# Kernel optimization log

Measured on AMD Instinct MI355X. Metric: run time of the kernel, lower is better.

## Reference

```python
import jax, jax.numpy as jnp
import numpy as np

B, S, D, H = 4, 2048, 1024, 16
DH = D // H
DFF = 4 * D
EPS = 1e-7


def _layernorm(x, scale, shift):
    # Note original quirk: (normalized + shift) * scale, biased variance, eps=1e-7
    m = jnp.mean(x, axis=-1, keepdims=True)
    v = jnp.mean((x - m) ** 2, axis=-1, keepdims=True)
    return ((x - m) / jnp.sqrt(v + EPS) + shift) * scale


def _gelu(x):
    c = jnp.sqrt(jnp.asarray(2.0 / jnp.pi, dtype=x.dtype))
    return 0.5 * x * (1.0 + jnp.tanh(c * (x + 0.044715 * x ** 3)))


def setup_inputs() -> dict:
    key = jax.random.key(0)
    ks = jax.random.split(key, 8)
    s = 0.02
    return {
        "x": jax.random.normal(ks[0], (B, S, D), jnp.float32),
        "Wq": jax.random.normal(ks[1], (D, D), jnp.float32) * s,
        "Wk": jax.random.normal(ks[2], (D, D), jnp.float32) * s,
        "Wv": jax.random.normal(ks[3], (D, D), jnp.float32) * s,
        "Wo": jax.random.normal(ks[4], (D, D), jnp.float32) * s,
        "bo": jnp.zeros((D,), jnp.float32),
        "W1": jax.random.normal(ks[5], (DFF, D), jnp.float32) * s,
        "b1": jnp.zeros((DFF,), jnp.float32),
        "W2": jax.random.normal(ks[6], (D, DFF), jnp.float32) * s,
        "b2": jnp.zeros((D,), jnp.float32),
        "ln1_scale": jnp.ones((D,), jnp.float32),
        "ln1_shift": jnp.zeros((D,), jnp.float32),
        "ln2_scale": jnp.ones((D,), jnp.float32),
        "ln2_shift": jnp.zeros((D,), jnp.float32),
    }


def reference(x, Wq, Wk, Wv, Wo, bo, W1, b1, W2, b2,
              ln1_scale, ln1_shift, ln2_scale, ln2_shift):
    b, s, d = x.shape
    h = _layernorm(x, ln1_scale, ln1_shift)
    # torch Linear: y = h @ W.T
    q = (h @ Wq.T).reshape(b, s, H, DH).transpose(0, 2, 1, 3)  # bhsd
    k = (h @ Wk.T).reshape(b, s, H, DH).transpose(0, 2, 1, 3)
    v = (h @ Wv.T).reshape(b, s, H, DH).transpose(0, 2, 1, 3)
    scores = jnp.einsum('bhqd,bhkd->bhqk', q, k) / jnp.sqrt(jnp.asarray(DH, x.dtype))
    causal = jnp.tril(jnp.ones((s, s), dtype=bool))
    scores = jnp.where(causal, scores, -jnp.inf)
    attn = jax.nn.softmax(scores, axis=-1)
    ctx = jnp.einsum('bhqk,bhkd->bhqd', attn, v)
    ctx = ctx.transpose(0, 2, 1, 3).reshape(b, s, d)
    attn_out = ctx @ Wo.T + bo
    x1 = x + attn_out  # residual (dropout is identity at eval / p effectively unused)
    h2 = _layernorm(x1, ln2_scale, ln2_shift)
    ff = _gelu(h2 @ W1.T + b1) @ W2.T + b2
    return x1 + ff
```

## Files before the change

kernel.cpp:

```cpp
#include <hip/hip_runtime.h>
#include <hip/hip_bf16.h>
#include <math.h>

typedef __bf16 bf16;
typedef __bf16 bf16x2_t __attribute__((ext_vector_type(2)));
typedef __bf16 bf16x4_t __attribute__((ext_vector_type(4)));
typedef __bf16 bf16x8_t __attribute__((ext_vector_type(8)));
typedef float  floatx4  __attribute__((ext_vector_type(4)));

#define DEVI static __device__ __forceinline__

constexpr int Bb = 4, Ss = 2048, Dd = 1024, Hh = 16, DHh = 64, DFFc = 4096;
constexpr int NTOK = Bb * Ss;
constexpr int NQKV = 3072;

DEVI void gld_lds16(const void* g, void* l) {
  __builtin_amdgcn_global_load_lds(
      (const __attribute__((address_space(1))) void*)g,
      (__attribute__((address_space(3))) void*)l, 16, 0, 0);
}

DEVI float gelu_f(float x) {
  const float c = 0.7978845608028654f;
  float t = tanhf(c * (x + 0.044715f * x * x * x));
  return 0.5f * x * (1.0f + t);
}

DEVI int xcd_lin(int lin, int nwg) {
  return (lin & 7) * (nwg >> 3) + (lin >> 3);
}

struct CastArgs {
  const float* src[6];
  bf16* dst[6];
  int n[6];
};
__global__ __launch_bounds__(256) void cast_w_kernel(CastArgs a) {
  const int which = blockIdx.y;
  const int idx = (blockIdx.x * 256 + threadIdx.x) * 4;
  if (idx >= a.n[which]) return;
  float4 v = *(const float4*)(a.src[which] + idx);
  bf16x4_t o = {(bf16)v.x, (bf16)v.y, (bf16)v.z, (bf16)v.w};
  *(bf16x4_t*)(a.dst[which] + idx) = o;
}

template <typename TIN>
__global__ __launch_bounds__(256) void ln_kernel(const TIN* __restrict__ x,
                                                 const float* __restrict__ sc,
                                                 const float* __restrict__ sh,
                                                 bf16* __restrict__ out) {
  __shared__ float rs[4], rs2[4];
  const int row = blockIdx.x, t = threadIdx.x;
  const TIN* xr = x + (size_t)row * Dd;
  float v[4];
  if constexpr (sizeof(TIN) == 2) {
    bf16x4_t tmp = *(const bf16x4_t*)((const bf16*)xr + t * 4);
#pragma unroll
    for (int i = 0; i < 4; i++) v[i] = (float)tmp[i];
  } else {
    float4 tmp = *(const float4*)((const float*)xr + t * 4);
    v[0] = tmp.x; v[1] = tmp.y; v[2] = tmp.z; v[3] = tmp.w;
  }
  float s = v[0] + v[1] + v[2] + v[3];
  float s2 = v[0] * v[0] + v[1] * v[1] + v[2] * v[2] + v[3] * v[3];
#pragma unroll
  for (int off = 1; off < 64; off <<= 1) {
    s += __shfl_xor(s, off);
    s2 += __shfl_xor(s2, off);
  }
  if ((t & 63) == 0) { rs[t >> 6] = s; rs2[t >> 6] = s2; }
  __syncthreads();
  float S1 = rs[0] + rs[1] + rs[2] + rs[3];
  float S2 = rs2[0] + rs2[1] + rs2[2] + rs2[3];
  float mean = S1 * (1.0f / Dd);
  float var = S2 * (1.0f / Dd) - mean * mean;
  float rinv = rsqrtf(var + 1e-7f);
#pragma unroll
  for (int i = 0; i < 4; i++) {
    int c = t * 4 + i;
    out[(size_t)row * Dd + c] = (bf16)(((v[i] - mean) * rinv + sh[c]) * sc[c]);
  }
}

template <int MODE>
__global__ __launch_bounds__(512, 2) void gemm8(const bf16* __restrict__ A,
                                                const bf16* __restrict__ Bw,
                                                const float* __restrict__ bias,
                                                const void* __restrict__ res,
                                                void* __restrict__ outp,
                                                int M, int N, int K) {
  constexpr int ABUF = 16384;
  constexpr int BBUF = 8192;
  __shared__ bf16 lds[3 * (ABUF + BBUF)];
  bf16* Ab = lds;
  bf16* Bb = lds + 3 * ABUF;

  const int tid = threadIdx.x;
  const int w = tid >> 6, lane = tid & 63;
  const int quad = lane >> 4, l16 = lane & 15;
  const int l7x8 = (lane & 7) << 3;
  const int wr = w >> 1, wc = w & 1;

  const int gx = (int)gridDim.x;
  const int nwg = gx * (int)gridDim.y;
  const int lin = xcd_lin((int)blockIdx.y * gx + (int)blockIdx.x, nwg);
  const int m0 = (lin / gx) * 256;
  const int n0 = (lin % gx) * 128;

  const int s0 = w * 1024 + lane * 16;
  const int sr = s0 >> 7;
  const int sc = ((s0 ^ ((sr & 7) << 4)) & 127) >> 1;
  const int toff = w * 512 + lane * 8;

  const bf16* Ag[2][2];
  const bf16* Bg[2];
#pragma unroll
  for (int h = 0; h < 2; h++)
#pragma unroll
    for (int j = 0; j < 2; j++)
      Ag[h][j] = A + (size_t)(m0 + h * 128 + j * 64 + sr) * K + sc;
#pragma unroll
  for (int j = 0; j < 2; j++)
    Bg[j] = Bw + (size_t)(n0 + j * 64 + sr) * K + sc;

  auto issue = [&](int kofs, int s) {
#pragma unroll
    for (int h = 0; h < 2; h++)
#pragma unroll
      for (int j = 0; j < 2; j++)
        gld_lds16(Ag[h][j] + kofs, Ab + s * ABUF + h * 8192 + j * 4096 + toff);
#pragma unroll
    for (int j = 0; j < 2; j++)
      gld_lds16(Bg[j] + kofs, Bb + s * BBUF + j * 4096 + toff);
  };

  const int abase = (wr * 64 + l16) * 64 + quad * 8;
  const int bbase = (wc * 64 + l16) * 64 + quad * 8;

  floatx4 acc[4][4] = {};

  const int NT = K >> 6;
  issue(0, 0);
  issue(64, 1);

  for (int t = 0; t < NT; ++t) {
    const int s = t % 3;
    if (t < NT - 1) {
      asm volatile("s_waitcnt vmcnt(6)" ::: "memory");
    } else {
      asm volatile("s_waitcnt vmcnt(0)" ::: "memory");
    }
    __builtin_amdgcn_sched_barrier(0);
    __builtin_amdgcn_s_barrier();
    __builtin_amdgcn_sched_barrier(0);
    if (t + 2 < NT) issue((t + 2) * 64, (t + 2) % 3);

    const bf16* aB = Ab + s * ABUF;
    const bf16* bB = Bb + s * BBUF;
    bf16x8_t bfr[4][2];
#pragma unroll
    for (int p = 0; p < 2; ++p) {
      bf16x8_t af[2][2];
#pragma unroll
      for (int im = 0; im < 2; ++im)
#pragma unroll
        for (int kk = 0; kk < 2; ++kk)
          af[im][kk] = *(const bf16x8_t*)(
              aB + ((abase + (p * 2 + im) * 1024 + kk * 32) ^ l7x8));
      if (p == 0) {
#pragma unroll
        for (int j2 = 0; j2 < 4; ++j2)
#pragma unroll
          for (int kk = 0; kk < 2; ++kk)
            bfr[j2][kk] = *(const bf16x8_t*)(
                bB + ((bbase + j2 * 1024 + kk * 32) ^ l7x8));
      }
      __builtin_amdgcn_s_barrier();
      __builtin_amdgcn_sched_barrier(0);
      __builtin_amdgcn_s_setprio(1);
#pragma unroll
      for (int im = 0; im < 2; ++im)
#pragma unroll
        for (int j2 = 0; j2 < 4; ++j2)
#pragma unroll
          for (int kk = 0; kk < 2; ++kk)
            acc[p * 2 + im][j2] = __builtin_amdgcn_mfma_f32_16x16x32_bf16(
                af[im][kk], bfr[j2][kk], acc[p * 2 + im][j2], 0, 0, 0);
      __builtin_amdgcn_s_setprio(0);
      if (p == 0) {
        __builtin_amdgcn_s_barrier();
        __builtin_amdgcn_sched_barrier(0);
      }
    }
  }

#pragma unroll
  for (int i = 0; i < 4; ++i) {
    const int rbase = m0 + wr * 64 + i * 16 + quad * 4;
#pragma unroll
    for (int j2 = 0; j2 < 4; ++j2) {
      const int col = n0 + wc * 64 + j2 * 16 + l16;
      float bv = 0.f;
      if constexpr (MODE == 1 || MODE == 2 || MODE == 3) bv = bias[col];
#pragma unroll
      for (int r = 0; r < 4; ++r) {
        const int row = rbase + r;
        float vacc = acc[i][j2][r] + bv;
        if constexpr (MODE == 0) {
          ((bf16*)outp)[(size_t)row * N + col] = (bf16)vacc;
        } else if constexpr (MODE == 1) {
          float xres = ((const float*)res)[(size_t)row * N + col];
          ((bf16*)outp)[(size_t)row * N + col] = (bf16)(xres + vacc);
        } else if constexpr (MODE == 2) {
          ((bf16*)outp)[(size_t)row * N + col] = (bf16)gelu_f(vacc);
        } else {
          float xres = (float)((const bf16*)res)[(size_t)row * N + col];
          ((float*)outp)[(size_t)row * N + col] = xres + vacc;
        }
      }
    }
  }
}

__global__ __launch_bounds__(256) void attn_kernel(const bf16* __restrict__ QKV,
                                                   bf16* __restrict__ ctx) {
  __shared__ bf16 Ks[64 * 72];
  __shared__ bf16 Vt[64 * 72];
  __shared__ bf16 Ps[4][16 * 72];

  const int tid = threadIdx.x;
  const int wave = tid >> 6, lane = tid & 63;
  const int quad = lane >> 4, l16 = lane & 15;
  const int lin = xcd_lin((int)blockIdx.y * 16 + (int)blockIdx.x, 16 * Bb * Hh);
  const int qb = lin & 15;
  const int bh = lin >> 4;
  const int bsel = bh >> 4, hsel = bh & 15;
  const size_t base = ((size_t)bsel * Ss) * NQKV + (size_t)hsel * 64;
  const bf16* Qp = QKV + base;
  const bf16* Kp = QKV + base + 1024;
  const bf16* Vp = QKV + base + 2048;

  const int kr0 = tid >> 3, kc0 = (tid & 7) * 8;
  const int vp2 = tid & 31, vs = tid >> 5;

  for (int t = 0; t < 2; t++) {
    const int qt = (t == 0) ? qb : 31 - qb;
    const int q0 = qt * 64;

    const int qrow = q0 + wave * 16 + l16;
    bf16x8_t qf0 = *(const bf16x8_t*)(Qp + (size_t)qrow * NQKV + quad * 8);
    bf16x8_t qf1 = *(const bf16x8_t*)(Qp + (size_t)qrow * NQKV + 32 + quad * 8);
#pragma unroll
    for (int i = 0; i < 8; i++) {
      qf0[i] = (bf16)((float)qf0[i] * 0.125f);
      qf1[i] = (bf16)((float)qf1[i] * 0.125f);
    }

    floatx4 o[4] = {};
    float l_i[4] = {0.f, 0.f, 0.f, 0.f};

    {
      bf16x8_t k0 = *(const bf16x8_t*)(Kp + (size_t)kr0 * NQKV + kc0);
      bf16x8_t k1 = *(const bf16x8_t*)(Kp + (size_t)(kr0 + 32) * NQKV + kc0);
      const bf16* v0p = Vp + (size_t)(2 * vp2) * NQKV + vs * 8;
      bf16x8_t va = *(const bf16x8_t*)(v0p);
      bf16x8_t vb = *(const bf16x8_t*)(v0p + NQKV);
      *(bf16x8_t*)(Ks + kr0 * 72 + kc0) = k0;
      *(bf16x8_t*)(Ks + (kr0 + 32) * 72 + kc0) = k1;
#pragma unroll
      for (int i = 0; i < 8; i++) {
        bf16x2_t p2 = {va[i], vb[i]};
        *(bf16x2_t*)(Vt + (vs * 8 + i) * 72 + 2 * vp2) = p2;
      }
      __syncthreads();
    }

    const int ntiles = qt + 1;
    for (int it = 0; it < ntiles; ++it) {
      const int kc = it * 64;
      const bool more = (it + 1) < ntiles;

      bf16x8_t nk0, nk1, nva, nvb;
      if (more) {
        const int kn = kc + 64;
        nk0 = *(const bf16x8_t*)(Kp + (size_t)(kn + kr0) * NQKV + kc0);
        nk1 = *(const bf16x8_t*)(Kp + (size_t)(kn + kr0 + 32) * NQKV + kc0);
        const bf16* v0p = Vp + (size_t)(kn + 2 * vp2) * NQKV + vs * 8;
        nva = *(const bf16x8_t*)(v0p);
        nvb = *(const bf16x8_t*)(v0p + NQKV);
      }

      floatx4 sg[4];
      __builtin_amdgcn_s_setprio(1);
#pragma unroll
      for (int g = 0; g < 4; g++) {
        floatx4 s = {0.f, 0.f, 0.f, 0.f};
        bf16x8_t ka = *(const bf16x8_t*)(Ks + (g * 16 + l16) * 72 + quad * 8);
        bf16x8_t kb = *(const bf16x8_t*)(Ks + (g * 16 + l16) * 72 + 32 + quad * 8);
        s = __builtin_amdgcn_mfma_f32_16x16x32_bf16(qf0, ka, s, 0, 0, 0);
        s = __builtin_amdgcn_mfma_f32_16x16x32_bf16(qf1, kb, s, 0, 0, 0);
        sg[g] = s;
      }
      __builtin_amdgcn_s_setprio(0);

      bf16* pw = &Ps[wave][0];
      const bool diag = (kc == q0);
      if (diag) {
#pragma unroll
        for (int r = 0; r < 4; r++) {
          const int rq = q0 + wave * 16 + quad * 4 + r;
          float p[4];
          float rsum = 0.f;
#pragma unroll
          for (int g = 0; g < 4; g++) {
            float v = (kc + g * 16 + l16 > rq) ? -1e30f : sg[g][r];
            p[g] = __expf(v);
            rsum += p[g];
          }
          rsum += __shfl_xor(rsum, 1);
          rsum += __shfl_xor(rsum, 2);
          rsum += __shfl_xor(rsum, 4);
          rsum += __shfl_xor(rsum, 8);
          l_i[r] += rsum;
#pragma unroll
          for (int g = 0; g < 4; g++)
            pw[(quad * 4 + r) * 72 + g * 16 + l16] = (bf16)p[g];
        }
      } else {
#pragma unroll
        for (int r = 0; r < 4; r++) {
          float p[4];
          float rsum = 0.f;
#pragma unroll
          for (int g = 0; g < 4; g++) {
            p[g] = __expf(sg[g][r]);
            rsum += p[g];
          }
          rsum += __shfl_xor(rsum, 1);
          rsum += __shfl_xor(rsum, 2);
          rsum += __shfl_xor(rsum, 4);
          rsum += __shfl_xor(rsum, 8);
          l_i[r] += rsum;
#pragma unroll
          for (int g = 0; g < 4; g++)
            pw[(quad * 4 + r) * 72 + g * 16 + l16] = (bf16)p[g];
        }
      }

      bf16x8_t pf0 = *(const bf16x8_t*)(pw + l16 * 72 + quad * 8);
      bf16x8_t pf1 = *(const bf16x8_t*)(pw + l16 * 72 + 32 + quad * 8);
      __builtin_amdgcn_s_setprio(1);
#pragma unroll
      for (int nt = 0; nt < 4; nt++) {
        bf16x8_t vf0 = *(const bf16x8_t*)(Vt + (nt * 16 + l16) * 72 + quad * 8);
        bf16x8_t vf1 = *(const bf16x8_t*)(Vt + (nt * 16 + l16) * 72 + 32 + quad * 8);
        o[nt] = __builtin_amdgcn_mfma_f32_16x16x32_bf16(pf0, vf0, o[nt], 0, 0, 0);
        o[nt] = __builtin_amdgcn_mfma_f32_16x16x32_bf16(pf1, vf1, o[nt], 0, 0, 0);
      }
      __builtin_amdgcn_s_setprio(0);

      __syncthreads();
      if (more) {
        *(bf16x8_t*)(Ks + kr0 * 72 + kc0) = nk0;
        *(bf16x8_t*)(Ks + (kr0 + 32) * 72 + kc0) = nk1;
#pragma unroll
        for (int i = 0; i < 8; i++) {
          bf16x2_t p2 = {nva[i], nvb[i]};
          *(bf16x2_t*)(Vt + (vs * 8 + i) * 72 + 2 * vp2) = p2;
        }
        __syncthreads();
      }
    }

#pragma unroll
    for (int nt = 0; nt < 4; nt++)
#pragma unroll
      for (int r = 0; r < 4; r++) {
        const int rq = q0 + wave * 16 + quad * 4 + r;
        size_t a = ((size_t)bsel * Ss + rq) * Dd + (size_t)hsel * DHh + nt * 16 + l16;
        ctx[a] = (bf16)(o[nt][r] / l_i[r]);
      }
  }
}

extern "C" void kernel_launch(void* const* d_in, const int* in_sizes, int n_in,
                              void* d_out, int out_size, void* d_ws, size_t ws_size,
                              hipStream_t stream) {
  (void)in_sizes; (void)n_in; (void)out_size; (void)ws_size;
  const float* x = (const float*)d_in[0];
  const float* Wq = (const float*)d_in[1];
  const float* Wk = (const float*)d_in[2];
  const float* Wv = (const float*)d_in[3];
  const float* Wo = (const float*)d_in[4];
  const float* bo = (const float*)d_in[5];
  const float* W1 = (const float*)d_in[6];
  const float* b1 = (const float*)d_in[7];
  const float* W2 = (const float*)d_in[8];
  const float* b2 = (const float*)d_in[9];
  const float* ln1s = (const float*)d_in[10];
  const float* ln1b = (const float*)d_in[11];
  const float* ln2s = (const float*)d_in[12];
  const float* ln2b = (const float*)d_in[13];

  char* wsb = (char*)d_ws;
  const size_t MB = 1024 * 1024;
  bf16* Wqb = (bf16*)(wsb);
  bf16* Wkb = (bf16*)(wsb + 2 * MB);
  bf16* Wvb = (bf16*)(wsb + 4 * MB);
  bf16* Wob = (bf16*)(wsb + 6 * MB);
  bf16* W1b = (bf16*)(wsb + 8 * MB);
  bf16* W2b = (bf16*)(wsb + 16 * MB);
  bf16* h   = (bf16*)(wsb + 24 * MB);
  bf16* qkv = (bf16*)(wsb + 40 * MB);
  bf16* ctx = (bf16*)(wsb + 88 * MB);
  bf16* x1  = (bf16*)(wsb + 104 * MB);
  bf16* h2  = ctx;
  bf16* ff1 = h;

  dim3 blk(256, 1, 1);
  dim3 blk8(512, 1, 1);

  CastArgs ca;
  ca.src[0] = Wq; ca.src[1] = Wk; ca.src[2] = Wv; ca.src[3] = Wo;
  ca.src[4] = W1; ca.src[5] = W2;
  ca.dst[0] = Wqb; ca.dst[1] = Wkb; ca.dst[2] = Wvb; ca.dst[3] = Wob;
  ca.dst[4] = W1b; ca.dst[5] = W2b;
  ca.n[0] = ca.n[1] = ca.n[2] = ca.n[3] = Dd * Dd;
  ca.n[4] = ca.n[5] = Dd * DFFc;
  cast_w_kernel<<<dim3((Dd * DFFc) / (256 * 4), 6, 1), blk, 0, stream>>>(ca);

  ln_kernel<float><<<dim3(NTOK, 1, 1), blk, 0, stream>>>(x, ln1s, ln1b, h);
  gemm8<0><<<dim3(24, NTOK / 256, 1), blk8, 0, stream>>>(h, Wqb, nullptr, nullptr,
                                                         qkv, NTOK, NQKV, Dd);
  attn_kernel<<<dim3(16, Bb * Hh, 1), blk, 0, stream>>>(qkv, ctx);
  gemm8<1><<<dim3(8, NTOK / 256, 1), blk8, 0, stream>>>(ctx, Wob, bo, x, x1,
                                                        NTOK, Dd, Dd);
  ln_kernel<bf16><<<dim3(NTOK, 1, 1), blk, 0, stream>>>(x1, ln2s, ln2b, h2);
  gemm8<2><<<dim3(32, NTOK / 256, 1), blk8, 0, stream>>>(h2, W1b, b1, nullptr, ff1,
                                                         NTOK, DFFc, Dd);
  gemm8<3><<<dim3(8, NTOK / 256, 1), blk8, 0, stream>>>(ff1, W2b, b2, x1,
                                                        (float*)d_out, NTOK, Dd, DFFc);
}
```

Measured before the change: 530.4 us.

## Template GEMM on tile width, use 256x256 tiles and split-phase double buffering

The GEMM kernel is templated on the N tile width. The QKV and FFN1 projections now use 256x256 block tiles with a 2x4 warp layout, which raises data reuse per loaded tile and halves the grid. LDS buffering drops from three stages to two, and global-to-LDS loads are split into halves issued at different phases of the MFMA loop, with waitcnt and barriers placed so that prefetch overlaps compute. The larger tiles raise LDS and register pressure and leave fewer workgroups to spread across CUs.

```diff
diff --git a/kernel.cpp b/kernel.cpp
--- a/kernel.cpp
+++ b/kernel.cpp
@@ -82,98 +82,111 @@
   }
 }
 
-template <int MODE>
-__global__ __launch_bounds__(512, 2) void gemm8(const bf16* __restrict__ A,
+template <int BN, int MODE>
+__global__ __launch_bounds__(512, 2) void gemmk(const bf16* __restrict__ A,
                                                 const bf16* __restrict__ Bw,
                                                 const float* __restrict__ bias,
                                                 const void* __restrict__ res,
                                                 void* __restrict__ outp,
                                                 int M, int N, int K) {
-  constexpr int ABUF = 16384;
-  constexpr int BBUF = 8192;
-  __shared__ bf16 lds[3 * (ABUF + BBUF)];
+  constexpr int BUNITS = BN / 64;
+  constexpr int AELEM = 16384;
+  constexpr int BELEM = BUNITS * 4096;
+  constexpr int WN = (BN == 256) ? 4 : 2;
+  constexpr int WM = 8 / WN;
+  constexpr int WR_H = 256 / WM;
+  constexpr int M_rep = WR_H / 16;
+  constexpr int NPH = M_rep / 2;
+  __shared__ bf16 lds[2 * (AELEM + BELEM)];
   bf16* Ab = lds;
-  bf16* Bb = lds + 3 * ABUF;
+  bf16* Bl = lds + 2 * AELEM;
 
   const int tid = threadIdx.x;
   const int w = tid >> 6, lane = tid & 63;
   const int quad = lane >> 4, l16 = lane & 15;
   const int l7x8 = (lane & 7) << 3;
-  const int wr = w >> 1, wc = w & 1;
+  const int wr = w / WN, wc = w % WN;
 
   const int gx = (int)gridDim.x;
   const int nwg = gx * (int)gridDim.y;
   const int lin = xcd_lin((int)blockIdx.y * gx + (int)blockIdx.x, nwg);
   const int m0 = (lin / gx) * 256;
-  const int n0 = (lin % gx) * 128;
+  const int n0 = (lin % gx) * BN;
 
   const int s0 = w * 1024 + lane * 16;
   const int sr = s0 >> 7;
   const int sc = ((s0 ^ ((sr & 7) << 4)) & 127) >> 1;
   const int toff = w * 512 + lane * 8;
 
-  const bf16* Ag[2][2];
-  const bf16* Bg[2];
-#pragma unroll
-  for (int h = 0; h < 2; h++)
-#pragma unroll
-    for (int j = 0; j < 2; j++)
-      Ag[h][j] = A + (size_t)(m0 + h * 128 + j * 64 + sr) * K + sc;
-#pragma unroll
-  for (int j = 0; j < 2; j++)
-    Bg[j] = Bw + (size_t)(n0 + j * 64 + sr) * K + sc;
-
-  auto issue = [&](int kofs, int s) {
-#pragma unroll
-    for (int h = 0; h < 2; h++)
-#pragma unroll
-      for (int j = 0; j < 2; j++)
-        gld_lds16(Ag[h][j] + kofs, Ab + s * ABUF + h * 8192 + j * 4096 + toff);
-#pragma unroll
-    for (int j = 0; j < 2; j++)
-      gld_lds16(Bg[j] + kofs, Bb + s * BBUF + j * 4096 + toff);
+  const bf16* Agu[4];
+  const bf16* Bgu[BUNITS];
+#pragma unroll
+  for (int u = 0; u < 4; ++u) Agu[u] = A + (size_t)(m0 + u * 64 + sr) * K + sc;
+#pragma unroll
+  for (int u = 0; u < BUNITS; ++u)
+    Bgu[u] = Bw + (size_t)(n0 + u * 64 + sr) * K + sc;
+
+  auto issA = [&](int t, int lo) {
+    const int q = t & 1, ko = t * 64;
+#pragma unroll
+    for (int u = 0; u < 2; ++u)
+      gld_lds16(Agu[lo + u] + ko, Ab + q * AELEM + (lo + u) * 4096 + toff);
   };
-
-  const int abase = (wr * 64 + l16) * 64 + quad * 8;
-  const int bbase = (wc * 64 + l16) * 64 + quad * 8;
-
-  floatx4 acc[4][4] = {};
-
+  auto issB = [&](int t, int lo, int cnt) {
+    const int q = t & 1, ko = t * 64;
+#pragma unroll 2
+    for (int u = 0; u < cnt; ++u)
+      gld_lds16(Bgu[lo + u] + ko, Bl + q * BELEM + (lo + u) * 4096 + toff);
+  };
+
+  auto rdA = [&](int q, int mi, int kk) {
+    const int r = wr * WR_H + mi * 16 + l16;
+    return *(const bf16x8_t*)(Ab + q * AELEM + (r >> 6) * 4096 + (r & 63) * 64 +
+                              ((quad * 8 + kk * 32) ^ l7x8));
+  };
+  auto rdB = [&](int q, int j, int kk) {
+    const int r = wc * 64 + j * 16 + l16;
+    return *(const bf16x8_t*)(Bl + q * BELEM + (r >> 6) * 4096 + (r & 63) * 64 +
+                              ((quad * 8 + kk * 32) ^ l7x8));
+  };
+
+  floatx4 acc[M_rep][4] = {};
   const int NT = K >> 6;
-  issue(0, 0);
-  issue(64, 1);
+
+  issA(0, 0); issA(0, 2); issB(0, 0, BUNITS);
+  issA(1, 0);
+  if (BN == 256) {
+    issB(1, 0, 2);
+    asm volatile("s_waitcnt vmcnt(4)" ::: "memory");
+  } else {
+    asm volatile("s_waitcnt vmcnt(2)" ::: "memory");
+  }
+  __builtin_amdgcn_sched_barrier(0);
+  __builtin_amdgcn_s_barrier();
+  __builtin_amdgcn_sched_barrier(0);
 
   for (int t = 0; t < NT; ++t) {
-    const int s = t % 3;
-    if (t < NT - 1) {
-      asm volatile("s_waitcnt vmcnt(6)" ::: "memory");
-    } else {
-      asm volatile("s_waitcnt vmcnt(0)" ::: "memory");
-    }
-    __builtin_amdgcn_sched_barrier(0);
-    __builtin_amdgcn_s_barrier();
-    __builtin_amdgcn_sched_barrier(0);
-    if (t + 2 < NT) issue((t + 2) * 64, (t + 2) % 3);
-
-    const bf16* aB = Ab + s * ABUF;
-    const bf16* bB = Bb + s * BBUF;
-    bf16x8_t bfr[4][2];
-#pragma unroll
-    for (int p = 0; p < 2; ++p) {
+    const int q = t & 1;
+    bf16x8_t bfv[4][2];
+#pragma unroll
+    for (int p = 0; p < NPH; ++p) {
       bf16x8_t af[2][2];
 #pragma unroll
       for (int im = 0; im < 2; ++im)
 #pragma unroll
         for (int kk = 0; kk < 2; ++kk)
-          af[im][kk] = *(const bf16x8_t*)(
-              aB + ((abase + (p * 2 + im) * 1024 + kk * 32) ^ l7x8));
+          af[im][kk] = rdA(q, p * 2 + im, kk);
       if (p == 0) {
 #pragma unroll
-        for (int j2 = 0; j2 < 4; ++j2)
+        for (int j = 0; j < 4; ++j)
 #pragma unroll
           for (int kk = 0; kk < 2; ++kk)
-            bfr[j2][kk] = *(const bf16x8_t*)(
-                bB + ((bbase + j2 * 1024 + kk * 32) ^ l7x8));
+            bfv[j][kk] = rdB(q, j, kk);
+        if (t + 1 < NT) {
+          issA(t + 1, 2);
+          if (BN == 256) issB(t + 1, 2, 2);
+          else issB(t + 1, 0, 2);
+        }
       }
       __builtin_amdgcn_s_barrier();
       __builtin_amdgcn_sched_barrier(0);
@@ -181,22 +194,31 @@
 #pragma unroll
       for (int im = 0; im < 2; ++im)
 #pragma unroll
-        for (int j2 = 0; j2 < 4; ++j2)
+        for (int j = 0; j < 4; ++j)
 #pragma unroll
           for (int kk = 0; kk < 2; ++kk)
-            acc[p * 2 + im][j2] = __builtin_amdgcn_mfma_f32_16x16x32_bf16(
-                af[im][kk], bfr[j2][kk], acc[p * 2 + im][j2], 0, 0, 0);
+            acc[p * 2 + im][j] = __builtin_amdgcn_mfma_f32_16x16x32_bf16(
+                af[im][kk], bfv[j][kk], acc[p * 2 + im][j], 0, 0, 0);
       __builtin_amdgcn_s_setprio(0);
-      if (p == 0) {
-        __builtin_amdgcn_s_barrier();
+      if (p == NPH - 1) {
+        if (t + 2 < NT) {
+          issA(t + 2, 0);
+          if (BN == 256) issB(t + 2, 0, 2);
+          if (BN == 256) asm volatile("s_waitcnt vmcnt(4)" ::: "memory");
+          else           asm volatile("s_waitcnt vmcnt(2)" ::: "memory");
+        } else {
+          asm volatile("s_waitcnt vmcnt(0)" ::: "memory");
+        }
         __builtin_amdgcn_sched_barrier(0);
       }
+      __builtin_amdgcn_s_barrier();
+      __builtin_amdgcn_sched_barrier(0);
     }
   }
 
 #pragma unroll
-  for (int i = 0; i < 4; ++i) {
-    const int rbase = m0 + wr * 64 + i * 16 + quad * 4;
+  for (int i = 0; i < M_rep; ++i) {
+    const int rbase = m0 + wr * WR_H + i * 16 + quad * 4;
 #pragma unroll
     for (int j2 = 0; j2 < 4; ++j2) {
       const int col = n0 + wc * 64 + j2 * 16 + l16;
@@ -430,14 +452,14 @@
   cast_w_kernel<<<dim3((Dd * DFFc) / (256 * 4), 6, 1), blk, 0, stream>>>(ca);
 
   ln_kernel<float><<<dim3(NTOK, 1, 1), blk, 0, stream>>>(x, ln1s, ln1b, h);
-  gemm8<0><<<dim3(24, NTOK / 256, 1), blk8, 0, stream>>>(h, Wqb, nullptr, nullptr,
-                                                         qkv, NTOK, NQKV, Dd);
+  gemmk<256, 0><<<dim3(12, NTOK / 256, 1), blk8, 0, stream>>>(h, Wqb, nullptr, nullptr,
+                                                              qkv, NTOK, NQKV, Dd);
   attn_kernel<<<dim3(16, Bb * Hh, 1), blk, 0, stream>>>(qkv, ctx);
-  gemm8<1><<<dim3(8, NTOK / 256, 1), blk8, 0, stream>>>(ctx, Wob, bo, x, x1,
-                                                        NTOK, Dd, Dd);
+  gemmk<128, 1><<<dim3(8, NTOK / 256, 1), blk8, 0, stream>>>(ctx, Wob, bo, x, x1,
+                                                             NTOK, Dd, Dd);
   ln_kernel<bf16><<<dim3(NTOK, 1, 1), blk, 0, stream>>>(x1, ln2s, ln2b, h2);
-  gemm8<2><<<dim3(32, NTOK / 256, 1), blk8, 0, stream>>>(h2, W1b, b1, nullptr, ff1,
-                                                         NTOK, DFFc, Dd);
-  gemm8<3><<<dim3(8, NTOK / 256, 1), blk8, 0, stream>>>(ff1, W2b, b2, x1,
-                                                        (float*)d_out, NTOK, Dd, DFFc);
-}
+  gemmk<256, 2><<<dim3(16, NTOK / 256, 1), blk8, 0, stream>>>(h2, W1b, b1, nullptr, ff1,
+                                                              NTOK, DFFc, Dd);
+  gemmk<128, 3><<<dim3(8, NTOK / 256, 1), blk8, 0, stream>>>(ff1, W2b, b2, x1,
+                                                             (float*)d_out, NTOK, Dd, DFFc);
+}
```

After: 506.9 us. 4.4% less time.
